# Performance work log

Measured on AMD Instinct MI355X. Metric: run time of the kernel, lower is better.

Reference implementation:

```python
import jax, jax.numpy as jnp
import numpy as np

B, L, D, FF = 4, 4096, 1024, 4096
EPS = 1e-06


def setup_inputs() -> dict:
    key = jax.random.key(0)
    ks = jax.random.split(key, 20)
    s_d = 1.0 / np.sqrt(D)
    s_ff = 1.0 / np.sqrt(FF)
    inp = {
        "x": jax.random.normal(ks[0], (B, L, D), jnp.float32),
        "hidden": jax.random.normal(ks[1], (B, D), jnp.float32),
        # sioconv linears (stored as [in, out])
        "w_ln_z": jax.random.normal(ks[2], (D, D), jnp.float32) * s_d,
        "b_ln_z": jnp.zeros((D,), jnp.float32),
        "w_dt": jax.random.normal(ks[3], (D, D), jnp.float32) * s_d,
        "b_dt": jnp.zeros((D,), jnp.float32),
        "w_y": jax.random.normal(ks[4], (D, D), jnp.float32) * s_d,
        "b_y": jnp.zeros((D,), jnp.float32),
        "w_y_act": jax.random.normal(ks[5], (D, D), jnp.float32) * s_d,
        "b_y_act": jnp.zeros((D,), jnp.float32),
        # FFN SwiGLU
        "w_fc": jax.random.normal(ks[6], (D, FF), jnp.float32) * s_d,
        "b_fc": jnp.zeros((FF,), jnp.float32),
        "w_fc_act": jax.random.normal(ks[7], (D, FF), jnp.float32) * s_d,
        "b_fc_act": jnp.zeros((FF,), jnp.float32),
        "w_out": jax.random.normal(ks[8], (FF, D), jnp.float32) * s_ff,
        "b_out": jnp.zeros((D,), jnp.float32),
        # RMSNorm gains
        "g_sio": jnp.ones((D,), jnp.float32),
        "g_ffn": jnp.ones((D,), jnp.float32),
    }
    return inp


def _rmsnorm(x, g):
    return x * jax.lax.rsqrt(jnp.mean(x * x, axis=-1, keepdims=True) + EPS) * g


def _sioconv(x, hidden, w_ln_z, b_ln_z, w_dt, b_dt, w_y, b_y, w_y_act, b_y_act):
    # x: [B,L,D], hidden: [B,D]
    ln_z = -jax.nn.softplus(-(x @ w_ln_z + b_ln_z))       # [B,L,D]
    dt = x @ w_dt + b_dt
    ln_da = -jax.nn.softplus(-dt)
    ln_o_da = -jax.nn.softplus(dt)
    ln_o_da_cumsum = jnp.cumsum(ln_o_da, axis=1)
    # inner-chunk: exp(logcumsumexp(ln_z + ln_da - cumsum) + cumsum)
    lse = jax.lax.cumlogsumexp(ln_z + ln_da - ln_o_da_cumsum, axis=1)
    h_inner = jnp.exp(lse + ln_o_da_cumsum)
    # cross-chunk: decay applied to incoming hidden state
    h_cross = jnp.exp(ln_o_da_cumsum) * hidden[:, None, :]
    h = h_inner + h_cross
    y = (h @ w_y + b_y) * jax.nn.silu(x @ w_y_act + b_y_act)
    return y, h


def _ffn(x, w_fc, b_fc, w_fc_act, b_fc_act, w_out, b_out):
    return (x @ w_fc + b_fc) * jax.nn.silu(x @ w_fc_act + b_fc_act) @ w_out + b_out


def reference(x, hidden, w_ln_z, b_ln_z, w_dt, b_dt, w_y, b_y, w_y_act, b_y_act,
              w_fc, b_fc, w_fc_act, b_fc_act, w_out, b_out, g_sio, g_ffn):
    x_res = x
    y, h = _sioconv(_rmsnorm(x, g_sio), hidden,
                    w_ln_z, b_ln_z, w_dt, b_dt, w_y, b_y, w_y_act, b_y_act)
    x = y + x_res  # dropout is identity (p=0 / eval)
    x_res = x
    x = _ffn(_rmsnorm(x, g_ffn), w_fc, b_fc, w_fc_act, b_fc_act, w_out, b_out) + x_res
    return (x, h)
```

## Files before the change

### kernel.cpp

```cpp
#include <hip/hip_runtime.h>
#include <stdint.h>

using u16 = unsigned short;
typedef __attribute__((ext_vector_type(8))) __bf16 bf16x8;
typedef __attribute__((ext_vector_type(4))) float f32x4;

#define DEV __device__ __forceinline__

static constexpr int kB = 4, kL = 4096, kD = 1024, kFF = 4096;
static constexpr int kM = kB * kL;
static constexpr int kLC = 256, kNC = kL / kLC;
static constexpr float kEPS = 1e-6f;

DEV u16 f2bf(float v) {
  union { float f; uint32_t u; } x; x.f = v;
  uint32_t r = x.u + 0x7FFFu + ((x.u >> 16) & 1u);
  return (u16)(r >> 16);
}
DEV float bf2f(u16 u) {
  union { uint32_t u; float f; } x; x.u = (uint32_t)u << 16; return x.f;
}
DEV float sigm(float x) { return 1.0f / (1.0f + __expf(-x)); }

DEV void gload_lds16(const void* g, void* l) {
  __builtin_amdgcn_global_load_lds(
      (const __attribute__((address_space(1))) void*)g,
      (__attribute__((address_space(3))) void*)l, 16, 0, 0);
}

__global__ __launch_bounds__(256) void wtrans_kernel(const float* __restrict__ in,
                                                     u16* __restrict__ out,
                                                     int K, int N) {
  __shared__ float t[32][33];
  const int n0 = blockIdx.x * 32, k0 = blockIdx.y * 32;
  const int tx = threadIdx.x, ty = threadIdx.y;
#pragma unroll
  for (int i = 0; i < 4; ++i)
    t[ty + i * 8][tx] = in[(size_t)(k0 + ty + i * 8) * N + (n0 + tx)];
  __syncthreads();
#pragma unroll
  for (int i = 0; i < 4; ++i)
    out[(size_t)(n0 + ty + i * 8) * K + (k0 + tx)] = f2bf(t[tx][ty + i * 8]);
}

__global__ __launch_bounds__(256) void wtrans_pair(const float* __restrict__ a,
                                                   const float* __restrict__ b,
                                                   u16* __restrict__ out,
                                                   int K, int Ncols) {
  __shared__ float t[32][33];
  const int n0 = blockIdx.x * 32, k0 = blockIdx.y * 32;
  const int sel = (n0 >> 5) & 1;
  const int c0 = (n0 >> 6) * 32;
  const float* __restrict__ src = sel ? b : a;
  const int tx = threadIdx.x, ty = threadIdx.y;
#pragma unroll
  for (int i = 0; i < 4; ++i)
    t[ty + i * 8][tx] = src[(size_t)(k0 + ty + i * 8) * Ncols + (c0 + tx)];
  __syncthreads();
#pragma unroll
  for (int i = 0; i < 4; ++i)
    out[(size_t)(n0 + ty + i * 8) * K + (k0 + tx)] = f2bf(t[tx][ty + i * 8]);
}

__global__ __launch_bounds__(256) void rmsnorm_kernel(const float* __restrict__ x,
                                                      const float* __restrict__ g,
                                                      u16* __restrict__ out) {
  const int row = blockIdx.x;
  const int t = threadIdx.x;
  const float4 v = ((const float4*)(x + (size_t)row * kD))[t];
  float ss = v.x * v.x + v.y * v.y + v.z * v.z + v.w * v.w;
#pragma unroll
  for (int o = 1; o < 64; o <<= 1) ss += __shfl_xor(ss, o, 64);
  __shared__ float red[4];
  if ((t & 63) == 0) red[t >> 6] = ss;
  __syncthreads();
  const float tot = red[0] + red[1] + red[2] + red[3];
  const float sc = rsqrtf(tot * (1.0f / kD) + kEPS);
  const float4 gv = ((const float4*)g)[t];
  const uint32_t lo = (uint32_t)f2bf(v.x * sc * gv.x) | ((uint32_t)f2bf(v.y * sc * gv.y) << 16);
  const uint32_t hi = (uint32_t)f2bf(v.z * sc * gv.z) | ((uint32_t)f2bf(v.w * sc * gv.w) << 16);
  *(uint2*)(out + (size_t)row * kD + t * 4) = make_uint2(lo, hi);
}

template <int MODE>
__global__ __launch_bounds__(512) void gemm256(
    const u16* __restrict__ A, const u16* __restrict__ Bt,
    const float* __restrict__ bias, const float* __restrict__ bias2,
    const u16* __restrict__ aux, int auxld,
    const float* __restrict__ res, float* __restrict__ Cf,
    u16* __restrict__ Cb, float* __restrict__ C2,
    int M, int N, int K) {
  __shared__ u16 sm[65536];
  const int tid = threadIdx.x;
  const int lane = tid & 63;
  const int wave = tid >> 6;
  const int wr = wave >> 2, wc = wave & 3;

  const int gx = gridDim.x;
  const int nwg = gx * gridDim.y;
  const int bid = blockIdx.y * gx + blockIdx.x;
  const int q = nwg >> 3, r = nwg & 7;
  const int xcd = bid & 7, idx0 = bid >> 3;
  const int wg = (xcd < r ? xcd * (q + 1) : r * (q + 1) + (xcd - r) * q) + idx0;
  const int m0 = (wg / gx) * 256, n0 = (wg % gx) * 256;

  const int NK = K >> 6;

  const int l8 = lane >> 3, l7 = lane & 7;
  const int rsub = wave * 8 + l8;
  const int kel = (l7 ^ l8) * 8;
  const size_t srcA = (size_t)(m0 + rsub) * K + kel;
  const size_t srcB = (size_t)(n0 + rsub) * K + kel;

  auto stage_half = [&](int kt, int half) {
    const int bsel = (kt & 1) * 32768;
    if (half < 2) {
      u16* d = sm + bsel + tid * 8 + half * 8192;
      const u16* s = A + srcA + (size_t)kt * 64 + (size_t)(half * 2) * 64 * K;
      gload_lds16(s, d);
      gload_lds16(s + (size_t)64 * K, d + 4096);
    } else {
      const int hh = half - 2;
      u16* d = sm + bsel + 16384 + tid * 8 + hh * 8192;
      const u16* s = Bt + srcB + (size_t)kt * 64 + (size_t)(hh * 2) * 64 * K;
      gload_lds16(s, d);
      gload_lds16(s + (size_t)64 * K, d + 4096);
    }
  };

  const int ra = lane & 15;
  const int kx0 = ((lane >> 4) ^ l7) * 8;
  const int kx1 = (((lane >> 4) + 4) ^ l7) * 8;

  f32x4 acc[8][4] = {};
  bf16x8 al[4][2], ah[4][2], bl[2][2], bh[2][2];

  stage_half(0, 0); stage_half(0, 1); stage_half(0, 2); stage_half(0, 3);
  if (NK > 1) { stage_half(1, 0); stage_half(1, 1); stage_half(1, 2); stage_half(1, 3); }
  asm volatile("s_waitcnt vmcnt(8)");
  asm volatile("s_barrier" ::: "memory");

  for (int h = 0; h < NK; ++h) {
    const u16* Az = sm + (h & 1) * 32768 + (wr * 128 + ra) * 64;
    const u16* Bz = sm + (h & 1) * 32768 + 16384 + (wc * 64 + ra) * 64;

#pragma unroll
    for (int mi = 0; mi < 4; ++mi) {
      al[mi][0] = *(const bf16x8*)(Az + mi * 16 * 64 + kx0);
      al[mi][1] = *(const bf16x8*)(Az + mi * 16 * 64 + kx1);
    }
#pragma unroll
    for (int ni = 0; ni < 2; ++ni) {
      bl[ni][0] = *(const bf16x8*)(Bz + ni * 16 * 64 + kx0);
      bl[ni][1] = *(const bf16x8*)(Bz + ni * 16 * 64 + kx1);
    }
    asm volatile("s_barrier" ::: "memory");
    asm volatile("s_waitcnt lgkmcnt(0)");
    __builtin_amdgcn_s_setprio(1);
#pragma unroll
    for (int mi = 0; mi < 4; ++mi)
#pragma unroll
      for (int ni = 0; ni < 2; ++ni)
#pragma unroll
        for (int kk = 0; kk < 2; ++kk)
          acc[mi][ni] = __builtin_amdgcn_mfma_f32_16x16x32_bf16(al[mi][kk], bl[ni][kk], acc[mi][ni], 0, 0, 0);
    __builtin_amdgcn_s_setprio(0);
    asm volatile("s_barrier" ::: "memory");

#pragma unroll
    for (int ni = 0; ni < 2; ++ni) {
      bh[ni][0] = *(const bf16x8*)(Bz + (32 + ni * 16) * 64 + kx0);
      bh[ni][1] = *(const bf16x8*)(Bz + (32 + ni * 16) * 64 + kx1);
    }
    asm volatile("s_barrier" ::: "memory");
    asm volatile("s_waitcnt lgkmcnt(0)");
    __builtin_amdgcn_s_setprio(1);
#pragma unroll
    for (int mi = 0; mi < 4; ++mi)
#pragma unroll
      for (int ni = 0; ni < 2; ++ni)
#pragma unroll
        for (int kk = 0; kk < 2; ++kk)
          acc[mi][2 + ni] = __builtin_amdgcn_mfma_f32_16x16x32_bf16(al[mi][kk], bh[ni][kk], acc[mi][2 + ni], 0, 0, 0);
    __builtin_amdgcn_s_setprio(0);
    asm volatile("s_barrier" ::: "memory");

#pragma unroll
    for (int mi = 0; mi < 4; ++mi) {
      ah[mi][0] = *(const bf16x8*)(Az + (64 + mi * 16) * 64 + kx0);
      ah[mi][1] = *(const bf16x8*)(Az + (64 + mi * 16) * 64 + kx1);
    }
    if (h + 2 < NK) { stage_half(h + 2, 2); stage_half(h + 2, 3); }
    asm volatile("s_barrier" ::: "memory");
    asm volatile("s_waitcnt lgkmcnt(0)");
    __builtin_amdgcn_s_setprio(1);
#pragma unroll
    for (int mi = 0; mi < 4; ++mi)
#pragma unroll
      for (int ni = 0; ni < 2; ++ni)
#pragma unroll
        for (int kk = 0; kk < 2; ++kk)
          acc[4 + mi][ni] = __builtin_amdgcn_mfma_f32_16x16x32_bf16(ah[mi][kk], bl[ni][kk], acc[4 + mi][ni], 0, 0, 0);
    __builtin_amdgcn_s_setprio(0);
    asm volatile("s_barrier" ::: "memory");

    if (h + 2 < NK) { stage_half(h + 2, 0); stage_half(h + 2, 1); }
    __builtin_amdgcn_s_setprio(1);
#pragma unroll
    for (int mi = 0; mi < 4; ++mi)
#pragma unroll
      for (int ni = 0; ni < 2; ++ni)
#pragma unroll
        for (int kk = 0; kk < 2; ++kk)
          acc[4 + mi][2 + ni] = __builtin_amdgcn_mfma_f32_16x16x32_bf16(ah[mi][kk], bh[ni][kk], acc[4 + mi][2 + ni], 0, 0, 0);
    __builtin_amdgcn_s_setprio(0);
    if (h + 2 < NK) asm volatile("s_waitcnt vmcnt(8)");
    else            asm volatile("s_waitcnt vmcnt(0)");
    asm volatile("s_barrier" ::: "memory");
  }

  const int ca = ra;
  const int rq = (lane >> 4) * 4;
  if (MODE == 6 || MODE == 7) {
    const int Nout = N >> 1;
#pragma unroll
    for (int mi = 0; mi < 8; ++mi) {
#pragma unroll
      for (int ni = 0; ni < 2; ++ni) {
        const int cout = (n0 >> 1) + wc * 32 + ni * 16 + ca;
        const float b1 = bias[cout], b2 = bias2[cout];
#pragma unroll
        for (int j = 0; j < 4; ++j) {
          const int rr = m0 + wr * 128 + mi * 16 + rq + j;
          const size_t idx = (size_t)rr * Nout + cout;
          const float v1 = acc[mi][ni][j] + b1;
          const float v2 = acc[mi][2 + ni][j] + b2;
          if (MODE == 7) {
            Cf[idx] = sigm(-v2);
            C2[idx] = sigm(v1) * sigm(v2);
          } else {
            Cb[idx] = f2bf(v2 * (v1 * sigm(v1)));
          }
        }
      }
    }
  } else {
#pragma unroll
    for (int mi = 0; mi < 8; ++mi) {
#pragma unroll
      for (int ni = 0; ni < 4; ++ni) {
        const int c = n0 + wc * 64 + ni * 16 + ca;
        const float bz = bias[c];
#pragma unroll
        for (int j = 0; j < 4; ++j) {
          const int rr = m0 + wr * 128 + mi * 16 + rq + j;
          const size_t idx = (size_t)rr * N + c;
          const float v = acc[mi][ni][j] + bz;
          if (MODE == 2) {
            const float a = bf2f(aux[(size_t)rr * auxld + c]);
            Cf[idx] = v * (a * sigm(a)) + res[idx];
          } else if (MODE == 4) {
            Cf[idx] = v + res[idx];
          } else {
            Cb[idx] = f2bf(v);
          }
        }
      }
    }
  }
}

__global__ __launch_bounds__(256) void scan_phase1(const float* __restrict__ Aa,
                                                   const float* __restrict__ Bv,
                                                   float* __restrict__ P,
                                                   float* __restrict__ S) {
  const int d = blockIdx.x * 256 + threadIdx.x;
  const int c = blockIdx.y, b = blockIdx.z;
  size_t base = ((size_t)b * kL + (size_t)c * kLC) * kD + d;
  float p = 1.0f, s = 0.0f;
#pragma unroll 4
  for (int l = 0; l < kLC; ++l) {
    const float a = Aa[base];
    const float bv = Bv[base];
    p *= a;
    s = fmaf(a, s, bv);
    base += kD;
  }
  const size_t o = ((size_t)b * kNC + c) * kD + d;
  P[o] = p; S[o] = s;
}

__global__ __launch_bounds__(256) void scan_phase2(const float* __restrict__ P,
                                                   const float* __restrict__ S,
                                                   const float* __restrict__ hidden,
                                                   float* __restrict__ Hini) {
  const int d = blockIdx.x * 256 + threadIdx.x;
  const int b = blockIdx.y;
  float carry = hidden[(size_t)b * kD + d];
  for (int c = 0; c < kNC; ++c) {
    const size_t o = ((size_t)b * kNC + c) * kD + d;
    Hini[o] = carry;
    carry = fmaf(P[o], carry, S[o]);
  }
}

__global__ __launch_bounds__(256) void scan_phase3(const float* __restrict__ Aa,
                                                   const float* __restrict__ Bv,
                                                   const float* __restrict__ Hini,
                                                   float* __restrict__ Hout,
                                                   u16* __restrict__ Hbf) {
  const int d = blockIdx.x * 256 + threadIdx.x;
  const int c = blockIdx.y, b = blockIdx.z;
  float h = Hini[((size_t)b * kNC + c) * kD + d];
  size_t base = ((size_t)b * kL + (size_t)c * kLC) * kD + d;
#pragma unroll 4
  for (int l = 0; l < kLC; ++l) {
    h = fmaf(Aa[base], h, Bv[base]);
    Hout[base] = h;
    Hbf[base] = f2bf(h);
    base += kD;
  }
}

extern "C" void kernel_launch(void* const* d_in, const int* in_sizes, int n_in,
                              void* d_out, int out_size, void* d_ws, size_t ws_size,
                              hipStream_t stream) {
  const float* x      = (const float*)d_in[0];
  const float* hidden = (const float*)d_in[1];
  const float* w_ln_z = (const float*)d_in[2];
  const float* b_ln_z = (const float*)d_in[3];
  const float* w_dt   = (const float*)d_in[4];
  const float* b_dt   = (const float*)d_in[5];
  const float* w_y    = (const float*)d_in[6];
  const float* b_y    = (const float*)d_in[7];
  const float* w_yact = (const float*)d_in[8];
  const float* b_yact = (const float*)d_in[9];
  const float* w_fc   = (const float*)d_in[10];
  const float* b_fc   = (const float*)d_in[11];
  const float* w_fca  = (const float*)d_in[12];
  const float* b_fca  = (const float*)d_in[13];
  const float* w_out  = (const float*)d_in[14];
  const float* b_out  = (const float*)d_in[15];
  const float* g_sio  = (const float*)d_in[16];
  const float* g_ffn  = (const float*)d_in[17];

  char* ws = (char*)d_ws;
  const size_t MiB = 1ull << 20;
  u16* wzdT  = (u16*)(ws + 0 * MiB);
  u16* wyaT  = (u16*)(ws + 4 * MiB);
  u16* wyT   = (u16*)(ws + 6 * MiB);
  u16* wfgT  = (u16*)(ws + 8 * MiB);
  u16* woutT = (u16*)(ws + 24 * MiB);
  u16*   xn    = (u16*)(ws + 33 * MiB);
  u16*   yabuf = (u16*)(ws + 65 * MiB);
  float* Abuf  = (float*)(ws + 97 * MiB);
  float* Bvbuf = (float*)(ws + 161 * MiB);
  u16*   hbf   = (u16*)(ws + 225 * MiB);
  u16*   Ubuf  = (u16*)(ws + 161 * MiB);
  float* Pbuf  = (float*)(ws + 289 * MiB);
  float* Sbuf  = (float*)(ws + 290 * MiB);
  float* Hini  = (float*)(ws + 291 * MiB);

  float* xout = (float*)d_out;
  float* hout = xout + (size_t)kM * kD;
  float* x1 = Abuf;

  const dim3 tb(32, 8);
  wtrans_pair<<<dim3(2048 / 32, kD / 32), tb, 0, stream>>>(w_ln_z, w_dt, wzdT, kD, kD);
  wtrans_pair<<<dim3(8192 / 32, kD / 32), tb, 0, stream>>>(w_fca, w_fc, wfgT, kD, kFF);
  wtrans_kernel<<<dim3(kD / 32, kD / 32), tb, 0, stream>>>(w_yact, wyaT, kD, kD);
  wtrans_kernel<<<dim3(kD / 32, kD / 32), tb, 0, stream>>>(w_y, wyT, kD, kD);
  wtrans_kernel<<<dim3(kD / 32, kFF / 32), tb, 0, stream>>>(w_out, woutT, kFF, kD);

  rmsnorm_kernel<<<kM, 256, 0, stream>>>(x, g_sio, xn);

  gemm256<7><<<dim3(2048 / 256, kM / 256), 512, 0, stream>>>(
      xn, wzdT, b_ln_z, b_dt, nullptr, 0, nullptr, Abuf, nullptr, Bvbuf, kM, 2048, kD);
  gemm256<5><<<dim3(kD / 256, kM / 256), 512, 0, stream>>>(
      xn, wyaT, b_yact, nullptr, nullptr, 0, nullptr, nullptr, yabuf, nullptr, kM, kD, kD);

  scan_phase1<<<dim3(kD / 256, kNC, kB), 256, 0, stream>>>(Abuf, Bvbuf, Pbuf, Sbuf);
  scan_phase2<<<dim3(kD / 256, kB), 256, 0, stream>>>(Pbuf, Sbuf, hidden, Hini);
  scan_phase3<<<dim3(kD / 256, kNC, kB), 256, 0, stream>>>(Abuf, Bvbuf, Hini, hout, hbf);

  gemm256<2><<<dim3(kD / 256, kM / 256), 512, 0, stream>>>(
      hbf, wyT, b_y, nullptr, yabuf, kD, x, x1, nullptr, nullptr, kM, kD, kD);

  rmsnorm_kernel<<<kM, 256, 0, stream>>>(x1, g_ffn, xn);

  gemm256<6><<<dim3(8192 / 256, kM / 256), 512, 0, stream>>>(
      xn, wfgT, b_fca, b_fc, nullptr, 0, nullptr, nullptr, Ubuf, nullptr, kM, 8192, kD);

  gemm256<4><<<dim3(kD / 256, kM / 256), 512, 0, stream>>>(
      Ubuf, woutT, b_out, nullptr, nullptr, 0, x1, xout, nullptr, nullptr, kM, kD, kFF);
}
```

Baseline: 776.3 us.

## Shrink GEMM tiles to 256x128 with BK=32 for higher occupancy

```diff
diff --git a/kernel.cpp b/kernel.cpp
--- a/kernel.cpp
+++ b/kernel.cpp
@@ -83,18 +83,18 @@
 }
 
 template <int MODE>
-__global__ __launch_bounds__(512) void gemm256(
+__global__ __launch_bounds__(512, 4) void gemm256(
     const u16* __restrict__ A, const u16* __restrict__ Bt,
     const float* __restrict__ bias, const float* __restrict__ bias2,
     const u16* __restrict__ aux, int auxld,
     const float* __restrict__ res, float* __restrict__ Cf,
     u16* __restrict__ Cb, float* __restrict__ C2,
     int M, int N, int K) {
-  __shared__ u16 sm[65536];
+  __shared__ u16 sm[24576];
   const int tid = threadIdx.x;
   const int lane = tid & 63;
   const int wave = tid >> 6;
-  const int wr = wave >> 2, wc = wave & 3;
+  const int wr = wave >> 1, wc = wave & 1;
 
   const int gx = gridDim.x;
   const int nwg = gx * gridDim.y;
@@ -102,58 +102,47 @@
   const int q = nwg >> 3, r = nwg & 7;
   const int xcd = bid & 7, idx0 = bid >> 3;
   const int wg = (xcd < r ? xcd * (q + 1) : r * (q + 1) + (xcd - r) * q) + idx0;
-  const int m0 = (wg / gx) * 256, n0 = (wg % gx) * 256;
-
-  const int NK = K >> 6;
-
-  const int l8 = lane >> 3, l7 = lane & 7;
-  const int rsub = wave * 8 + l8;
-  const int kel = (l7 ^ l8) * 8;
+  const int per = gridDim.y * 4;
+  const int sg = wg / per, srem = wg % per;
+  const int m0 = (srem >> 2) * 256;
+  const int n0 = (sg * 4 + (srem & 3)) * 128;
+
+  const int NK = K >> 5;
+
+  const int rsub = wave * 16 + (lane >> 2);
+  const int kel = ((((lane >> 2) ^ lane) & 3)) * 8;
   const size_t srcA = (size_t)(m0 + rsub) * K + kel;
   const size_t srcB = (size_t)(n0 + rsub) * K + kel;
 
-  auto stage_half = [&](int kt, int half) {
-    const int bsel = (kt & 1) * 32768;
-    if (half < 2) {
-      u16* d = sm + bsel + tid * 8 + half * 8192;
-      const u16* s = A + srcA + (size_t)kt * 64 + (size_t)(half * 2) * 64 * K;
-      gload_lds16(s, d);
-      gload_lds16(s + (size_t)64 * K, d + 4096);
-    } else {
-      const int hh = half - 2;
-      u16* d = sm + bsel + 16384 + tid * 8 + hh * 8192;
-      const u16* s = Bt + srcB + (size_t)kt * 64 + (size_t)(hh * 2) * 64 * K;
-      gload_lds16(s, d);
-      gload_lds16(s + (size_t)64 * K, d + 4096);
-    }
+  auto stageA = [&](int kt) {
+    u16* d = sm + (kt & 1) * 12288 + tid * 8;
+    const u16* s = A + srcA + (size_t)kt * 32;
+    gload_lds16(s, d);
+    gload_lds16(s + (size_t)128 * K, d + 4096);
   };
-
-  const int ra = lane & 15;
-  const int kx0 = ((lane >> 4) ^ l7) * 8;
-  const int kx1 = (((lane >> 4) + 4) ^ l7) * 8;
-
-  f32x4 acc[8][4] = {};
-  bf16x8 al[4][2], ah[4][2], bl[2][2], bh[2][2];
-
-  stage_half(0, 0); stage_half(0, 1); stage_half(0, 2); stage_half(0, 3);
-  if (NK > 1) { stage_half(1, 0); stage_half(1, 1); stage_half(1, 2); stage_half(1, 3); }
-  asm volatile("s_waitcnt vmcnt(8)");
+  auto stageB = [&](int kt) {
+    gload_lds16(Bt + srcB + (size_t)kt * 32,
+                sm + (kt & 1) * 12288 + 8192 + tid * 8);
+  };
+
+  const int rb = (lane & 15) * 32 + ((((lane >> 4) ^ lane) & 3) << 3);
+
+  f32x4 acc[4][4] = {};
+  bf16x8 af[4], bf[4];
+
+  stageA(0); stageB(0);
+  if (NK > 1) { stageA(1); stageB(1); }
+  asm volatile("s_waitcnt vmcnt(3)");
   asm volatile("s_barrier" ::: "memory");
 
   for (int h = 0; h < NK; ++h) {
-    const u16* Az = sm + (h & 1) * 32768 + (wr * 128 + ra) * 64;
-    const u16* Bz = sm + (h & 1) * 32768 + 16384 + (wc * 64 + ra) * 64;
-
-#pragma unroll
-    for (int mi = 0; mi < 4; ++mi) {
-      al[mi][0] = *(const bf16x8*)(Az + mi * 16 * 64 + kx0);
-      al[mi][1] = *(const bf16x8*)(Az + mi * 16 * 64 + kx1);
-    }
-#pragma unroll
-    for (int ni = 0; ni < 2; ++ni) {
-      bl[ni][0] = *(const bf16x8*)(Bz + ni * 16 * 64 + kx0);
-      bl[ni][1] = *(const bf16x8*)(Bz + ni * 16 * 64 + kx1);
-    }
+    const u16* Az = sm + (h & 1) * 12288 + wr * 2048;
+    const u16* Bz = sm + (h & 1) * 12288 + 8192 + wc * 2048;
+
+#pragma unroll
+    for (int mi = 0; mi < 4; ++mi) af[mi] = *(const bf16x8*)(Az + mi * 512 + rb);
+    bf[0] = *(const bf16x8*)(Bz + rb);
+    bf[1] = *(const bf16x8*)(Bz + 512 + rb);
     asm volatile("s_barrier" ::: "memory");
     asm volatile("s_waitcnt lgkmcnt(0)");
     __builtin_amdgcn_s_setprio(1);
@@ -161,77 +150,46 @@
     for (int mi = 0; mi < 4; ++mi)
 #pragma unroll
       for (int ni = 0; ni < 2; ++ni)
-#pragma unroll
-        for (int kk = 0; kk < 2; ++kk)
-          acc[mi][ni] = __builtin_amdgcn_mfma_f32_16x16x32_bf16(al[mi][kk], bl[ni][kk], acc[mi][ni], 0, 0, 0);
+        acc[mi][ni] = __builtin_amdgcn_mfma_f32_16x16x32_bf16(af[mi], bf[ni], acc[mi][ni], 0, 0, 0);
     __builtin_amdgcn_s_setprio(0);
     asm volatile("s_barrier" ::: "memory");
 
-#pragma unroll
-    for (int ni = 0; ni < 2; ++ni) {
-      bh[ni][0] = *(const bf16x8*)(Bz + (32 + ni * 16) * 64 + kx0);
-      bh[ni][1] = *(const bf16x8*)(Bz + (32 + ni * 16) * 64 + kx1);
-    }
+    bf[2] = *(const bf16x8*)(Bz + 1024 + rb);
+    bf[3] = *(const bf16x8*)(Bz + 1536 + rb);
+    if (h + 2 < NK) stageA(h + 2);
     asm volatile("s_barrier" ::: "memory");
     asm volatile("s_waitcnt lgkmcnt(0)");
     __builtin_amdgcn_s_setprio(1);
 #pragma unroll
     for (int mi = 0; mi < 4; ++mi)
-#pragma unroll
-      for (int ni = 0; ni < 2; ++ni)
-#pragma unroll
-        for (int kk = 0; kk < 2; ++kk)
-          acc[mi][2 + ni] = __builtin_amdgcn_mfma_f32_16x16x32_bf16(al[mi][kk], bh[ni][kk], acc[mi][2 + ni], 0, 0, 0);
+      acc[mi][2] = __builtin_amdgcn_mfma_f32_16x16x32_bf16(af[mi], bf[2], acc[mi][2], 0, 0, 0);
     __builtin_amdgcn_s_setprio(0);
     asm volatile("s_barrier" ::: "memory");
 
-#pragma unroll
-    for (int mi = 0; mi < 4; ++mi) {
-      ah[mi][0] = *(const bf16x8*)(Az + (64 + mi * 16) * 64 + kx0);
-      ah[mi][1] = *(const bf16x8*)(Az + (64 + mi * 16) * 64 + kx1);
-    }
-    if (h + 2 < NK) { stage_half(h + 2, 2); stage_half(h + 2, 3); }
-    asm volatile("s_barrier" ::: "memory");
-    asm volatile("s_waitcnt lgkmcnt(0)");
+    if (h + 2 < NK) stageB(h + 2);
     __builtin_amdgcn_s_setprio(1);
 #pragma unroll
     for (int mi = 0; mi < 4; ++mi)
-#pragma unroll
-      for (int ni = 0; ni < 2; ++ni)
-#pragma unroll
-        for (int kk = 0; kk < 2; ++kk)
-          acc[4 + mi][ni] = __builtin_amdgcn_mfma_f32_16x16x32_bf16(ah[mi][kk], bl[ni][kk], acc[4 + mi][ni], 0, 0, 0);
+      acc[mi][3] = __builtin_amdgcn_mfma_f32_16x16x32_bf16(af[mi], bf[3], acc[mi][3], 0, 0, 0);
     __builtin_amdgcn_s_setprio(0);
-    asm volatile("s_barrier" ::: "memory");
-
-    if (h + 2 < NK) { stage_half(h + 2, 0); stage_half(h + 2, 1); }
-    __builtin_amdgcn_s_setprio(1);
-#pragma unroll
-    for (int mi = 0; mi < 4; ++mi)
-#pragma unroll
-      for (int ni = 0; ni < 2; ++ni)
-#pragma unroll
-        for (int kk = 0; kk < 2; ++kk)
-          acc[4 + mi][2 + ni] = __builtin_amdgcn_mfma_f32_16x16x32_bf16(ah[mi][kk], bh[ni][kk], acc[4 + mi][2 + ni], 0, 0, 0);
-    __builtin_amdgcn_s_setprio(0);
-    if (h + 2 < NK) asm volatile("s_waitcnt vmcnt(8)");
+    if (h + 2 < NK) asm volatile("s_waitcnt vmcnt(3)");
     else            asm volatile("s_waitcnt vmcnt(0)");
     asm volatile("s_barrier" ::: "memory");
   }
 
-  const int ca = ra;
+  const int ca = lane & 15;
   const int rq = (lane >> 4) * 4;
   if (MODE == 6 || MODE == 7) {
     const int Nout = N >> 1;
 #pragma unroll
-    for (int mi = 0; mi < 8; ++mi) {
+    for (int mi = 0; mi < 4; ++mi) {
 #pragma unroll
       for (int ni = 0; ni < 2; ++ni) {
         const int cout = (n0 >> 1) + wc * 32 + ni * 16 + ca;
         const float b1 = bias[cout], b2 = bias2[cout];
 #pragma unroll
         for (int j = 0; j < 4; ++j) {
-          const int rr = m0 + wr * 128 + mi * 16 + rq + j;
+          const int rr = m0 + wr * 64 + mi * 16 + rq + j;
           const size_t idx = (size_t)rr * Nout + cout;
           const float v1 = acc[mi][ni][j] + b1;
           const float v2 = acc[mi][2 + ni][j] + b2;
@@ -246,14 +204,14 @@
     }
   } else {
 #pragma unroll
-    for (int mi = 0; mi < 8; ++mi) {
+    for (int mi = 0; mi < 4; ++mi) {
 #pragma unroll
       for (int ni = 0; ni < 4; ++ni) {
         const int c = n0 + wc * 64 + ni * 16 + ca;
         const float bz = bias[c];
 #pragma unroll
         for (int j = 0; j < 4; ++j) {
-          const int rr = m0 + wr * 128 + mi * 16 + rq + j;
+          const int rr = m0 + wr * 64 + mi * 16 + rq + j;
           const size_t idx = (size_t)rr * N + c;
           const float v = acc[mi][ni][j] + bz;
           if (MODE == 2) {
@@ -374,23 +332,23 @@
 
   rmsnorm_kernel<<<kM, 256, 0, stream>>>(x, g_sio, xn);
 
-  gemm256<7><<<dim3(2048 / 256, kM / 256), 512, 0, stream>>>(
+  gemm256<7><<<dim3(2048 / 128, kM / 256), 512, 0, stream>>>(
       xn, wzdT, b_ln_z, b_dt, nullptr, 0, nullptr, Abuf, nullptr, Bvbuf, kM, 2048, kD);
-  gemm256<5><<<dim3(kD / 256, kM / 256), 512, 0, stream>>>(
+  gemm256<5><<<dim3(kD / 128, kM / 256), 512, 0, stream>>>(
       xn, wyaT, b_yact, nullptr, nullptr, 0, nullptr, nullptr, yabuf, nullptr, kM, kD, kD);
 
   scan_phase1<<<dim3(kD / 256, kNC, kB), 256, 0, stream>>>(Abuf, Bvbuf, Pbuf, Sbuf);
   scan_phase2<<<dim3(kD / 256, kB), 256, 0, stream>>>(Pbuf, Sbuf, hidden, Hini);
   scan_phase3<<<dim3(kD / 256, kNC, kB), 256, 0, stream>>>(Abuf, Bvbuf, Hini, hout, hbf);
 
-  gemm256<2><<<dim3(kD / 256, kM / 256), 512, 0, stream>>>(
+  gemm256<2><<<dim3(kD / 128, kM / 256), 512, 0, stream>>>(
       hbf, wyT, b_y, nullptr, yabuf, kD, x, x1, nullptr, nullptr, kM, kD, kD);
 
   rmsnorm_kernel<<<kM, 256, 0, stream>>>(x1, g_ffn, xn);
 
-  gemm256<6><<<dim3(8192 / 256, kM / 256), 512, 0, stream>>>(
+  gemm256<6><<<dim3(8192 / 128, kM / 256), 512, 0, stream>>>(
       xn, wfgT, b_fca, b_fc, nullptr, 0, nullptr, nullptr, Ubuf, nullptr, kM, 8192, kD);
 
-  gemm256<4><<<dim3(kD / 256, kM / 256), 512, 0, stream>>>(
+  gemm256<4><<<dim3(kD / 128, kM / 256), 512, 0, stream>>>(
       Ubuf, woutT, b_out, nullptr, nullptr, 0, x1, xout, nullptr, nullptr, kM, kD, kFF);
 }
```

New measurement: 802.9 us. +3.4%, slower.
